# Kernel optimization log

Hardware: AMD Instinct MI355X
Metric: run time of the kernel (lower is better)

## Reference

```python
import jax, jax.numpy as jnp
import numpy as np

N, E, D, G, L = 100000, 1600000, 128, 64, 3


def _layernorm(h, g, b, eps=1e-5):
    mu = jnp.mean(h, axis=-1, keepdims=True)
    var = jnp.var(h, axis=-1, keepdims=True)
    return (h - mu) * jax.lax.rsqrt(var + eps) * g + b


def setup_inputs() -> dict:
    key = jax.random.key(0)
    ks = jax.random.split(key, 10)
    s = 1.0 / np.sqrt(D)
    return {
        "x": jax.random.normal(ks[0], (N, D), dtype=jnp.float32),
        "edge_index": jax.random.randint(ks[1], (2, E), 0, N, dtype=jnp.int64),
        "batch": jnp.sort(jax.random.randint(ks[2], (N,), 0, G, dtype=jnp.int64)),
        "fc_w": jax.random.normal(ks[3], (D, D), dtype=jnp.float32) * s,
        "fc_b": jnp.zeros((D,), dtype=jnp.float32),
        "w_self": jax.random.normal(ks[4], (L, D, D), dtype=jnp.float32) * s,
        "w_neigh": jax.random.normal(ks[5], (L, D, D), dtype=jnp.float32) * s,
        "conv_b": jnp.zeros((L, D), dtype=jnp.float32),
        "ln_g": jnp.ones((L, D), dtype=jnp.float32),
        "ln_b": jnp.zeros((L, D), dtype=jnp.float32),
    }


def reference(x, edge_index, batch, fc_w, fc_b, w_self, w_neigh, conv_b, ln_g, ln_b):
    src, dst = edge_index[0], edge_index[1]
    # in-degree for mean aggregation (clamped to avoid div-by-zero)
    deg = jax.ops.segment_sum(jnp.ones((E,), dtype=x.dtype), dst, num_segments=N)
    deg = jnp.maximum(deg, 1.0)[:, None]  # [N,1]

    node = x @ fc_w + fc_b                      # input projection
    graph = jnp.zeros((G, D), dtype=x.dtype)    # initial graph embed (None -> 0)

    for l in range(L):
        # SAGEConv: self transform + mean neighbor aggregation
        agg = jax.ops.segment_sum(node[src], dst, num_segments=N) / deg  # [N,D]
        h = node @ w_self[l] + agg @ w_neigh[l] + conv_b[l]
        g = jax.ops.segment_sum(h, batch, num_segments=G)  # graph_aggr='add'
        # residual (channel_match=True)
        h = h + node
        g = g + graph
        # norm + act (original applies norm twice to graph_out, no relu on it)
        node = jax.nn.relu(_layernorm(h, ln_g[l], ln_b[l]))
        graph = _layernorm(_layernorm(g, ln_g[l], ln_b[l]), ln_g[l], ln_b[l])
    return node, graph
```

## Files before the change

kernel.cpp:

```cpp
#include <hip/hip_runtime.h>

#define D 128
#define NG 64
#define NL 3
#define NPART 8

typedef __attribute__((ext_vector_type(8))) short bf16x8;
typedef __attribute__((ext_vector_type(4))) float f32x4;
typedef unsigned short u16;
typedef unsigned int   u32;

__device__ __forceinline__ u16 f2bf(float x) {
  u32 u = __float_as_uint(x);
  return (u16)((u + 0x7FFF + ((u >> 16) & 1)) >> 16);
}
__device__ __forceinline__ float bf2f(u16 b) {
  return __uint_as_float((u32)b << 16);
}

__global__ void k_count(const int* __restrict__ dst, int* __restrict__ cnt,
                        int E, int psize) {
  const int myp = blockIdx.x & (NPART - 1);
  const int lo  = myp * psize, hi = lo + psize;
  const int tpp = (gridDim.x / NPART) * blockDim.x;
  int i = (blockIdx.x >> 3) * blockDim.x + threadIdx.x;
  for (; i < E; i += tpp) {
    int t = __builtin_nontemporal_load(&dst[i]);
    if (t >= lo && t < hi) atomicAdd(&cnt[t], 1);
  }
}

__global__ void k_fill(const int* __restrict__ src, const int* __restrict__ dst,
                       int* __restrict__ cursor, int* __restrict__ csr_src,
                       int E, int psize) {
  const int myp = blockIdx.x & (NPART - 1);
  const int lo  = myp * psize, hi = lo + psize;
  const int tpp = (gridDim.x / NPART) * blockDim.x;
  int i = (blockIdx.x >> 3) * blockDim.x + threadIdx.x;
  for (; i < E; i += tpp) {
    int t = __builtin_nontemporal_load(&dst[i]);
    int s = __builtin_nontemporal_load(&src[i]);
    if (t >= lo && t < hi) {
      int pos = atomicAdd(&cursor[t], 1);
      csr_src[pos] = s;
    }
  }
}

__global__ void k_invdeg(const int* __restrict__ cnt, float* __restrict__ invdeg, int n) {
  int i = blockIdx.x * blockDim.x + threadIdx.x;
  if (i < n) invdeg[i] = 1.0f / (float)max(cnt[i], 1);
}

__global__ void k_blocksum(const int* __restrict__ cnt, int* __restrict__ bsum, int n) {
  int b = blockIdx.x, t = threadIdx.x;
  int base = b * 1024 + t * 4;
  int s = 0;
#pragma unroll
  for (int j = 0; j < 4; ++j) if (base + j < n) s += cnt[base + j];
  int lane = t & 63, w = t >> 6;
#pragma unroll
  for (int m = 1; m < 64; m <<= 1) s += __shfl_xor(s, m);
  __shared__ int ws[4];
  if (lane == 0) ws[w] = s;
  __syncthreads();
  if (t == 0) bsum[b] = ws[0] + ws[1] + ws[2] + ws[3];
}

__global__ void k_scan_bsum(int* __restrict__ bsum, int nb) {
  __shared__ int s[1024];
  int t = threadIdx.x;
  int v = t < nb ? bsum[t] : 0;
  s[t] = v;
  __syncthreads();
  for (int off = 1; off < 1024; off <<= 1) {
    int x = (t >= off) ? s[t - off] : 0;
    __syncthreads();
    s[t] += x;
    __syncthreads();
  }
  if (t < nb) bsum[t] = s[t] - v;
}

__global__ void k_rowptr(const int* __restrict__ cnt, const int* __restrict__ bsum,
                         int* __restrict__ rowptr, int* __restrict__ cursor, int n) {
  int b = blockIdx.x, t = threadIdx.x;
  int base = b * 1024 + t * 4;
  int v0 = 0, v1 = 0, v2 = 0, v3 = 0;
  if (base + 0 < n) v0 = cnt[base + 0];
  if (base + 1 < n) v1 = cnt[base + 1];
  if (base + 2 < n) v2 = cnt[base + 2];
  if (base + 3 < n) v3 = cnt[base + 3];
  int ts = v0 + v1 + v2 + v3;
  int lane = t & 63, w = t >> 6;
  int incl = ts;
#pragma unroll
  for (int m = 1; m < 64; m <<= 1) {
    int o = __shfl_up(incl, m);
    if (lane >= m) incl += o;
  }
  __shared__ int wsum[4];
  if (lane == 63) wsum[w] = incl;
  __syncthreads();
  int woff = 0;
  for (int i = 0; i < w; ++i) woff += wsum[i];
  int run = incl - ts + woff + bsum[b];
  if (base + 0 < n) { rowptr[base + 0] = run; cursor[base + 0] = run; run += v0; }
  if (base + 1 < n) { rowptr[base + 1] = run; cursor[base + 1] = run; run += v1; }
  if (base + 2 < n) { rowptr[base + 2] = run; cursor[base + 2] = run; run += v2; }
  if (base + 3 < n) { rowptr[base + 3] = run; cursor[base + 3] = run; run += v3; }
}

__global__ void k_wprep(const float* __restrict__ W, u16* __restrict__ Wt, int nmats) {
  long idx = (long)blockIdx.x * blockDim.x + threadIdx.x;
  long total = (long)nmats * 16384;
  long stride = (long)gridDim.x * blockDim.x;
  for (; idx < total; idx += stride) {
    long m = idx >> 14;
    int o = (int)(idx & 16383);
    int nn = o >> 7, k = o & 127;
    Wt[idx] = f2bf(W[m * 16384 + k * 128 + nn]);
  }
}

__global__ void k_aggr(const u16* __restrict__ nodeB,
                       const int* __restrict__ rowptr, const int* __restrict__ rowend,
                       const float* __restrict__ invdeg,
                       const int* __restrict__ csr_src,
                       u16* __restrict__ aggB, int n) {
  const int tid  = threadIdx.x;
  const int lane = tid & 63;
  const int l15  = lane & 15;
  const int g    = lane >> 4;
  const int wav  = (blockIdx.x * blockDim.x + tid) >> 6;
  const int node = wav * 4 + g;
  if (node >= n) return;

  const int s0 = rowptr[node];
  const int nk = rowend[node] - s0;
  const long off = (long)l15 * 8;

  float acc[8] = {};

  for (int kb = 0; kb < nk; kb += 16) {
    const int rem = min(16, nk - kb);
    int myidx = (l15 < rem) ? csr_src[s0 + kb + l15] : 0;
    int kk = 0;
    for (; kk + 8 <= rem; kk += 8) {
      bf16x8 v[8];
#pragma unroll
      for (int j = 0; j < 8; ++j) {
        int s = __shfl(myidx, (g << 4) + kk + j);
        v[j] = *(const bf16x8*)&nodeB[(long)s * D + off];
      }
#pragma unroll
      for (int j = 0; j < 8; ++j)
#pragma unroll
        for (int e = 0; e < 8; ++e)
          acc[e] += bf2f((u16)v[j][e]);
    }
    for (; kk + 4 <= rem; kk += 4) {
      bf16x8 v[4];
#pragma unroll
      for (int j = 0; j < 4; ++j) {
        int s = __shfl(myidx, (g << 4) + kk + j);
        v[j] = *(const bf16x8*)&nodeB[(long)s * D + off];
      }
#pragma unroll
      for (int j = 0; j < 4; ++j)
#pragma unroll
        for (int e = 0; e < 8; ++e)
          acc[e] += bf2f((u16)v[j][e]);
    }
    for (; kk < rem; ++kk) {
      int s = __shfl(myidx, (g << 4) + kk);
      bf16x8 v = *(const bf16x8*)&nodeB[(long)s * D + off];
#pragma unroll
      for (int e = 0; e < 8; ++e) acc[e] += bf2f((u16)v[e]);
    }
  }

  const float sc = invdeg[node];
  bf16x8 ov;
#pragma unroll
  for (int e = 0; e < 8; ++e) ov[e] = (short)f2bf(acc[e] * sc);
  *(bf16x8*)&aggB[(long)node * D + off] = ov;
}

__global__ __launch_bounds__(256) void k_proj_mfma(
    const float* __restrict__ X, const u16* __restrict__ WT,
    const float* __restrict__ bias, u16* __restrict__ OutB, int n)
{
  const int tid  = threadIdx.x;
  const int lane = tid & 63;
  const int w    = tid >> 6;
  const int l15  = lane & 15;
  const int g    = lane >> 4;
  const long base = (long)blockIdx.x * 64;

  long arow  = base + w * 16 + l15;
  long arowc = arow < n ? arow : (n - 1);

  bf16x8 aX[4];
#pragma unroll
  for (int ks = 0; ks < 4; ++ks) {
    int k0 = ks * 32 + g * 8;
    float4 x0 = *(const float4*)&X[arowc * D + k0];
    float4 x1 = *(const float4*)&X[arowc * D + k0 + 4];
    bf16x8 a;
    a[0] = (short)f2bf(x0.x); a[1] = (short)f2bf(x0.y);
    a[2] = (short)f2bf(x0.z); a[3] = (short)f2bf(x0.w);
    a[4] = (short)f2bf(x1.x); a[5] = (short)f2bf(x1.y);
    a[6] = (short)f2bf(x1.z); a[7] = (short)f2bf(x1.w);
    aX[ks] = a;
  }

  f32x4 acc[8] = {};
#pragma unroll
  for (int f = 0; f < 8; ++f) {
    int nn = f * 16 + l15;
#pragma unroll
    for (int ks = 0; ks < 4; ++ks) {
      int k0 = ks * 32 + g * 8;
      bf16x8 bW = *(const bf16x8*)&WT[nn * D + k0];
      acc[f] = __builtin_amdgcn_mfma_f32_16x16x32_bf16(aX[ks], bW, acc[f], 0, 0, 0);
    }
  }

  float bs[8];
#pragma unroll
  for (int f = 0; f < 8; ++f) bs[f] = bias[f * 16 + l15];

#pragma unroll
  for (int r = 0; r < 4; ++r) {
    long row = base + w * 16 + g * 4 + r;
    if (row >= n) continue;
#pragma unroll
    for (int f = 0; f < 8; ++f)
      OutB[row * D + f * 16 + l15] = f2bf(acc[f][r] + bs[f]);
  }
}

__global__ __launch_bounds__(512, 4) void k_conv_mfma(
    const u16* __restrict__ nodeB, const u16* __restrict__ aggB,
    const u16* __restrict__ WsT, const u16* __restrict__ WnT,
    const float* __restrict__ bias,
    const float* __restrict__ lg, const float* __restrict__ lb,
    const int* __restrict__ batch,
    float* __restrict__ gacc,
    u16* __restrict__ nodeOutB, float* __restrict__ nodeOutF,
    int n)
{
  __shared__ u16 w_lds[2 * D * D];
  __shared__ int batch_lds[128];
  const int tid  = threadIdx.x;
  const int lane = tid & 63;
  const int w    = tid >> 6;
  const int l15  = lane & 15;
  const int g    = lane >> 4;
  const long base = (long)blockIdx.x * 128;

  if (tid < 128) {
    long r = base + tid;
    batch_lds[tid] = batch[r < n ? r : (n - 1)];
  }

  long arow  = base + w * 16 + l15;
  long arowc = arow < n ? arow : (n - 1);
  bf16x8 aS[4], aA[4];
#pragma unroll
  for (int ks = 0; ks < 4; ++ks) {
    int k0 = ks * 32 + g * 8;
    aS[ks] = *(const bf16x8*)&nodeB[arowc * D + k0];
    aA[ks] = *(const bf16x8*)&aggB [arowc * D + k0];
  }

#pragma unroll
  for (int it = 0; it < 8; ++it) {
    int c    = it * 512 + tid;
    int row  = c >> 4;
    int col8 = c & 15;
    const u16* src = (c < 2048) ? &WsT[(long)c * 8] : &WnT[(long)(c - 2048) * 8];
    bf16x8 v = *(const bf16x8*)src;
    *(bf16x8*)&w_lds[row * D + (((col8) ^ (row & 15)) << 3)] = v;
  }
  __syncthreads();

  f32x4 acc[8] = {};
#pragma unroll
  for (int f = 0; f < 8; ++f) {
    const int wrow = f * 16 + l15;
#pragma unroll
    for (int ks = 0; ks < 4; ++ks) {
      const int cs = ((ks * 4 + g) ^ l15) << 3;
      bf16x8 bS = *(const bf16x8*)&w_lds[wrow * D + cs];
      bf16x8 bA = *(const bf16x8*)&w_lds[D * D + wrow * D + cs];
      acc[f] = __builtin_amdgcn_mfma_f32_16x16x32_bf16(aS[ks], bS, acc[f], 0, 0, 0);
      acc[f] = __builtin_amdgcn_mfma_f32_16x16x32_bf16(aA[ks], bA, acc[f], 0, 0, 0);
    }
  }

  float bs[8], lgv[8], lbv[8];
#pragma unroll
  for (int f = 0; f < 8; ++f) {
    bs[f]  = bias[f * 16 + l15];
    lgv[f] = lg[f * 16 + l15];
    lbv[f] = lb[f * 16 + l15];
  }
#pragma unroll
  for (int f = 0; f < 8; ++f)
#pragma unroll
    for (int r = 0; r < 4; ++r) acc[f][r] += bs[f];

  long rowb[4];
  bool valid[4];
#pragma unroll
  for (int r = 0; r < 4; ++r) {
    rowb[r]  = base + w * 16 + g * 4 + r;
    valid[r] = rowb[r] < n;
  }

  const int wb = w * 16;
  int b_first = batch_lds[wb], b_last = batch_lds[wb + 15];
  if (b_first == b_last) {
#pragma unroll
    for (int f = 0; f < 8; ++f) {
      float ps = 0.f;
#pragma unroll
      for (int r = 0; r < 4; ++r) if (valid[r]) ps += acc[f][r];
      ps += __shfl_xor(ps, 16);
      ps += __shfl_xor(ps, 32);
      if (lane < 16) atomicAdd(&gacc[b_first * D + f * 16 + lane], ps);
    }
  } else {
    int i = 0;
    while (i < 16) {
      int bseg = batch_lds[wb + i];
      int j = i + 1;
      while (j < 16 && batch_lds[wb + j] == bseg) ++j;
#pragma unroll
      for (int f = 0; f < 8; ++f) {
        float ps = 0.f;
#pragma unroll
        for (int r = 0; r < 4; ++r) {
          int lr = g * 4 + r;
          if (valid[r] && lr >= i && lr < j) ps += acc[f][r];
        }
        ps += __shfl_xor(ps, 16);
        ps += __shfl_xor(ps, 32);
        if (lane < 16) atomicAdd(&gacc[bseg * D + f * 16 + lane], ps);
      }
      i = j;
    }
  }

  float xv[8][4];
  float s[4] = {0, 0, 0, 0}, q[4] = {0, 0, 0, 0};
#pragma unroll
  for (int r = 0; r < 4; ++r) {
    long row = valid[r] ? rowb[r] : (n - 1);
#pragma unroll
    for (int f = 0; f < 8; ++f) {
      float nv = bf2f(nodeB[row * D + f * 16 + l15]);
      float x  = acc[f][r] + nv;
      xv[f][r] = x;
      s[r] += x; q[r] += x * x;
    }
  }
#pragma unroll
  for (int r = 0; r < 4; ++r) {
#pragma unroll
    for (int m = 1; m < 16; m <<= 1) {
      s[r] += __shfl_xor(s[r], m);
      q[r] += __shfl_xor(q[r], m);
    }
  }
#pragma unroll
  for (int r = 0; r < 4; ++r) {
    if (!valid[r]) continue;
    float mean = s[r] * (1.f / 128.f);
    float var  = q[r] * (1.f / 128.f) - mean * mean;
    float rs   = rsqrtf(fmaxf(var, 0.f) + 1e-5f);
#pragma unroll
    for (int f = 0; f < 8; ++f) {
      float y = fmaxf((xv[f][r] - mean) * rs * lgv[f] + lbv[f], 0.f);
      if (nodeOutB) nodeOutB[rowb[r] * D + f * 16 + l15] = f2bf(y);
      if (nodeOutF) nodeOutF[rowb[r] * D + f * 16 + l15] = y;
    }
  }
}

__global__ void k_ln_graph(const float* __restrict__ gacc,
                           float* __restrict__ graph,
                           const float* __restrict__ lg,
                           const float* __restrict__ lb)
{
  int row  = blockIdx.x;
  int lane = threadIdx.x;
  float2 gv = *(const float2*)&lg[lane * 2];
  float2 bv = *(const float2*)&lb[lane * 2];
  float2 a = *(const float2*)&gacc[row * D + lane * 2];
  float2 p = *(const float2*)&graph[row * D + lane * 2];
  float x0 = a.x + p.x, x1 = a.y + p.y;
#pragma unroll
  for (int pass = 0; pass < 2; ++pass) {
    float s = x0 + x1, q = x0 * x0 + x1 * x1;
#pragma unroll
    for (int m = 1; m < 64; m <<= 1) { s += __shfl_xor(s, m); q += __shfl_xor(q, m); }
    float mean = s * (1.f / 128.f);
    float var  = q * (1.f / 128.f) - mean * mean;
    float rs   = rsqrtf(fmaxf(var, 0.f) + 1e-5f);
    x0 = (x0 - mean) * rs * gv.x + bv.x;
    x1 = (x1 - mean) * rs * gv.y + bv.y;
  }
  float2 o; o.x = x0; o.y = x1;
  *(float2*)&graph[row * D + lane * 2] = o;
}

extern "C" void kernel_launch(void* const* d_in, const int* in_sizes, int n_in,
                              void* d_out, int out_size, void* d_ws, size_t ws_size,
                              hipStream_t stream)
{
  const float* x       = (const float*)d_in[0];
  const int*   edge    = (const int*)d_in[1];
  const int*   batch   = (const int*)d_in[2];
  const float* fc_w    = (const float*)d_in[3];
  const float* fc_b    = (const float*)d_in[4];
  const float* w_self  = (const float*)d_in[5];
  const float* w_neigh = (const float*)d_in[6];
  const float* conv_b  = (const float*)d_in[7];
  const float* ln_g    = (const float*)d_in[8];
  const float* ln_b    = (const float*)d_in[9];

  const int N = in_sizes[0] / D;
  const int E = in_sizes[1] / 2;
  const int* src = edge;
  const int* dst = edge + E;

  int*   cnt      = (int*)d_ws;
  int*   rowptr   = cnt + N;
  int*   cursor   = rowptr + N;
  int*   bsum     = cursor + N;
  int*   csr_src  = bsum + 1024;
  float* invdeg   = (float*)(csr_src + E);
  float* gacc     = invdeg + N;
  float* graphbuf = gacc + NG * D;
  char*  bfbase   = (char*)(graphbuf + NG * D);
  bfbase = (char*)(((size_t)bfbase + 15) & ~(size_t)15);
  u16*   nodeB    = (u16*)bfbase;
  u16*   aggB     = nodeB + (long)N * D;
  u16*   wsT      = aggB + (long)N * D;
  u16*   wnT      = wsT + 3 * D * D;
  u16*   fcT      = wnT + 3 * D * D;

  const int nb = (N + 1023) / 1024;
  const int psize = (N + NPART - 1) / NPART;

  hipMemsetAsync(cnt, 0, (size_t)N * sizeof(int), stream);
  hipMemsetAsync(graphbuf, 0, (size_t)NG * D * sizeof(float), stream);

  k_count<<<2048, 256, 0, stream>>>(dst, cnt, E, psize);
  k_invdeg<<<(N + 255) / 256, 256, 0, stream>>>(cnt, invdeg, N);
  k_blocksum<<<nb, 256, 0, stream>>>(cnt, bsum, N);
  k_scan_bsum<<<1, 1024, 0, stream>>>(bsum, nb);
  k_rowptr<<<nb, 256, 0, stream>>>(cnt, bsum, rowptr, cursor, N);
  k_fill<<<2048, 256, 0, stream>>>(src, dst, cursor, csr_src, E, psize);

  k_wprep<<<192, 256, 0, stream>>>(w_self,  wsT, NL);
  k_wprep<<<192, 256, 0, stream>>>(w_neigh, wnT, NL);
  k_wprep<<<64, 256, 0, stream>>>(fc_w, fcT, 1);

  const int pblocks = (N + 63) / 64;
  k_proj_mfma<<<pblocks, 256, 0, stream>>>(x, fcT, fc_b, nodeB, N);

  const int cblocks = (N + 127) / 128;
  const int ablocks = (N + 15) / 16;
  for (int l = 0; l < NL; ++l) {
    hipMemsetAsync(gacc, 0, (size_t)NG * D * sizeof(float), stream);
    k_aggr<<<ablocks, 256, 0, stream>>>(nodeB, rowptr, cursor, invdeg,
                                        csr_src, aggB, N);
    const bool last = (l == NL - 1);
    k_conv_mfma<<<cblocks, 512, 0, stream>>>(
        nodeB, aggB, wsT + (long)l * D * D, wnT + (long)l * D * D,
        conv_b + l * D, ln_g + l * D, ln_b + l * D,
        batch, gacc,
        last ? nullptr : nodeB, last ? (float*)d_out : nullptr, N);
    k_ln_graph<<<NG, 64, 0, stream>>>(gacc, graphbuf, ln_g + l * D, ln_b + l * D);
  }

  hipMemcpyAsync((float*)d_out + (long)N * D, graphbuf,
                 (size_t)NG * D * sizeof(float),
                 hipMemcpyDeviceToDevice, stream);
}
```

Measured before the change: 484.4 us.

## Pre-bucket edges by destination partition before CSR count and fill

The old count and fill kernels each scanned all edges once per partition (8 partitions), filtering by destination range. Edges are now counted per partition, then scattered once into a staged buffer grouped by partition, with LDS buffering so writes go out in coalesced 64-entry chunks of packed (dst,src) pairs. The local count and fill kernels then read only their partition's slice, which removes the redundant full-edge rereads. The cost is two extra kernels, a 12.8 MB staging buffer, and many block-level syncs in the bucketing loop.

```diff
diff --git a/kernel.cpp b/kernel.cpp
--- a/kernel.cpp
+++ b/kernel.cpp
@@ -9,6 +9,7 @@
 typedef __attribute__((ext_vector_type(4))) float f32x4;
 typedef unsigned short u16;
 typedef unsigned int   u32;
+typedef unsigned long long u64;
 
 __device__ __forceinline__ u16 f2bf(float x) {
   u32 u = __float_as_uint(x);
@@ -18,32 +19,104 @@
   return __uint_as_float((u32)b << 16);
 }
 
-__global__ void k_count(const int* __restrict__ dst, int* __restrict__ cnt,
-                        int E, int psize) {
-  const int myp = blockIdx.x & (NPART - 1);
-  const int lo  = myp * psize, hi = lo + psize;
-  const int tpp = (gridDim.x / NPART) * blockDim.x;
-  int i = (blockIdx.x >> 3) * blockDim.x + threadIdx.x;
-  for (; i < E; i += tpp) {
-    int t = __builtin_nontemporal_load(&dst[i]);
-    if (t >= lo && t < hi) atomicAdd(&cnt[t], 1);
-  }
-}
-
-__global__ void k_fill(const int* __restrict__ src, const int* __restrict__ dst,
-                       int* __restrict__ cursor, int* __restrict__ csr_src,
-                       int E, int psize) {
-  const int myp = blockIdx.x & (NPART - 1);
-  const int lo  = myp * psize, hi = lo + psize;
-  const int tpp = (gridDim.x / NPART) * blockDim.x;
-  int i = (blockIdx.x >> 3) * blockDim.x + threadIdx.x;
-  for (; i < E; i += tpp) {
-    int t = __builtin_nontemporal_load(&dst[i]);
-    int s = __builtin_nontemporal_load(&src[i]);
-    if (t >= lo && t < hi) {
-      int pos = atomicAdd(&cursor[t], 1);
-      csr_src[pos] = s;
-    }
+__global__ void k_pcount(const int* __restrict__ dst, int* __restrict__ pcnt,
+                         int E, int psize) {
+  __shared__ int lc[NPART];
+  if (threadIdx.x < NPART) lc[threadIdx.x] = 0;
+  __syncthreads();
+  int i = blockIdx.x * blockDim.x + threadIdx.x;
+  int stride = gridDim.x * blockDim.x;
+  for (; i < E; i += stride)
+    atomicAdd(&lc[__builtin_nontemporal_load(&dst[i]) / psize], 1);
+  __syncthreads();
+  if (threadIdx.x < NPART) atomicAdd(&pcnt[threadIdx.x], lc[threadIdx.x]);
+}
+
+__global__ void k_scan8(const int* __restrict__ pcnt, int* __restrict__ pbase,
+                        int* __restrict__ pfill) {
+  if (threadIdx.x == 0) {
+    int run = 0;
+    for (int p = 0; p < NPART; ++p) { pbase[p] = run; pfill[p] = run; run += pcnt[p]; }
+  }
+}
+
+__global__ __launch_bounds__(256) void k_bucket(
+    const int* __restrict__ src, const int* __restrict__ dst,
+    u64* __restrict__ staged, int* __restrict__ pfill, int E, int psize) {
+  __shared__ u64 buf[NPART][320];
+  __shared__ int bcnt[NPART];
+  __shared__ int gbase[NPART];
+  const int tid = threadIdx.x;
+  if (tid < NPART) bcnt[tid] = 0;
+  __syncthreads();
+
+  const int total_chunks = (E + 255) / 256;
+  for (int c = blockIdx.x; c < total_chunks; c += gridDim.x) {
+    int i = c * 256 + tid;
+    if (i < E) {
+      int t = __builtin_nontemporal_load(&dst[i]);
+      int s = __builtin_nontemporal_load(&src[i]);
+      int p = t / psize;
+      u64 pk = ((u64)(u32)t << 32) | (u32)s;
+      int slot = atomicAdd(&bcnt[p], 1);
+      buf[p][slot] = pk;
+    }
+    __syncthreads();
+    for (int q = 0; q < NPART; ++q) {
+      int cq = bcnt[q];
+      int f  = cq & ~63;
+      if (f > 0) {
+        if (tid == 0) gbase[q] = atomicAdd(&pfill[q], f);
+        __syncthreads();
+        int gb = gbase[q];
+        for (int j = tid; j < f; j += 256) staged[gb + j] = buf[q][j];
+        __syncthreads();
+        int rem = cq - f;
+        if (tid < rem) buf[q][tid] = buf[q][f + tid];
+        __syncthreads();
+        if (tid == 0) bcnt[q] = rem;
+        __syncthreads();
+      }
+    }
+    __syncthreads();
+  }
+  for (int q = 0; q < NPART; ++q) {
+    int cq = bcnt[q];
+    if (cq > 0) {
+      if (tid == 0) gbase[q] = atomicAdd(&pfill[q], cq);
+      __syncthreads();
+      int gb = gbase[q];
+      for (int j = tid; j < cq; j += 256) staged[gb + j] = buf[q][j];
+    }
+    __syncthreads();
+  }
+}
+
+__global__ void k_lcount(const u64* __restrict__ staged,
+                         const int* __restrict__ pbase, const int* __restrict__ pcnt,
+                         int* __restrict__ cnt) {
+  int p  = blockIdx.x & (NPART - 1);
+  int nb = gridDim.x >> 3;
+  int bi = blockIdx.x >> 3;
+  int lo = pbase[p], ce = pcnt[p];
+  for (int j = bi * blockDim.x + threadIdx.x; j < ce; j += nb * blockDim.x) {
+    u64 pk = staged[lo + j];
+    atomicAdd(&cnt[(int)(pk >> 32)], 1);
+  }
+}
+
+__global__ void k_lfill(const u64* __restrict__ staged,
+                        const int* __restrict__ pbase, const int* __restrict__ pcnt,
+                        int* __restrict__ cursor, int* __restrict__ csr_src) {
+  int p  = blockIdx.x & (NPART - 1);
+  int nb = gridDim.x >> 3;
+  int bi = blockIdx.x >> 3;
+  int lo = pbase[p], ce = pcnt[p];
+  for (int j = bi * blockDim.x + threadIdx.x; j < ce; j += nb * blockDim.x) {
+    u64 pk = staged[lo + j];
+    int t = (int)(pk >> 32);
+    int pos = atomicAdd(&cursor[t], 1);
+    csr_src[pos] = (int)(u32)pk;
   }
 }
 
@@ -441,7 +514,10 @@
   int*   rowptr   = cnt + N;
   int*   cursor   = rowptr + N;
   int*   bsum     = cursor + N;
-  int*   csr_src  = bsum + 1024;
+  int*   pcnt     = bsum + 1024;
+  int*   pbase    = pcnt + NPART;
+  int*   pfill    = pbase + NPART;
+  int*   csr_src  = pfill + NPART;
   float* invdeg   = (float*)(csr_src + E);
   float* gacc     = invdeg + N;
   float* graphbuf = gacc + NG * D;
@@ -452,19 +528,26 @@
   u16*   wsT      = aggB + (long)N * D;
   u16*   wnT      = wsT + 3 * D * D;
   u16*   fcT      = wnT + 3 * D * D;
+  char*  stb      = (char*)(fcT + D * D);
+  stb = (char*)(((size_t)stb + 7) & ~(size_t)7);
+  u64*   staged   = (u64*)stb;
 
   const int nb = (N + 1023) / 1024;
   const int psize = (N + NPART - 1) / NPART;
 
   hipMemsetAsync(cnt, 0, (size_t)N * sizeof(int), stream);
+  hipMemsetAsync(pcnt, 0, NPART * sizeof(int), stream);
   hipMemsetAsync(graphbuf, 0, (size_t)NG * D * sizeof(float), stream);
 
-  k_count<<<2048, 256, 0, stream>>>(dst, cnt, E, psize);
+  k_pcount<<<2048, 256, 0, stream>>>(dst, pcnt, E, psize);
+  k_scan8<<<1, 64, 0, stream>>>(pcnt, pbase, pfill);
+  k_bucket<<<2048, 256, 0, stream>>>(src, dst, staged, pfill, E, psize);
+  k_lcount<<<2048, 256, 0, stream>>>(staged, pbase, pcnt, cnt);
   k_invdeg<<<(N + 255) / 256, 256, 0, stream>>>(cnt, invdeg, N);
   k_blocksum<<<nb, 256, 0, stream>>>(cnt, bsum, N);
   k_scan_bsum<<<1, 1024, 0, stream>>>(bsum, nb);
   k_rowptr<<<nb, 256, 0, stream>>>(cnt, bsum, rowptr, cursor, N);
-  k_fill<<<2048, 256, 0, stream>>>(src, dst, cursor, csr_src, E, psize);
+  k_lfill<<<2048, 256, 0, stream>>>(staged, pbase, pcnt, cursor, csr_src);
 
   k_wprep<<<192, 256, 0, stream>>>(w_self,  wsT, NL);
   k_wprep<<<192, 256, 0, stream>>>(w_neigh, wnT, NL);
```

Result: slower. 967.2 us (+99.7%).
